# Kernel optimization log

Measured on AMD Instinct MI355X. Metric: run time of the kernel, lower is better.

The kernel has to match this reference:

```python
import jax, jax.numpy as jnp
import numpy as np

N = 100000      # nodes
E = 1600000     # edges (avg degree 16)
DIN = 32        # input feature dim
H = 16          # nhidden
DEPTH = 4       # number of SAGEConv layers


def setup_inputs() -> dict:
    key = jax.random.key(0)
    ks = jax.random.split(key, 16)
    s = 0.1
    inp = {
        "x": jax.random.normal(ks[0], (N, DIN), jnp.float32),
        "edge_index": jax.random.randint(ks[1], (2, E), 0, N, dtype=jnp.int64),
        # SAGEConv layer 0: in=DIN -> out=H. lin_l has bias, lin_r has no bias (PyG default).
        "Wl0": jax.random.normal(ks[2], (H, DIN), jnp.float32) * s,
        "bl0": jnp.zeros((H,), jnp.float32),
        "Wr0": jax.random.normal(ks[3], (H, DIN), jnp.float32) * s,
        # SAGEConv layers 1..3: in=H -> out=H, stacked.
        "Wls": jax.random.normal(ks[4], (DEPTH - 1, H, H), jnp.float32) * s,
        "bls": jnp.zeros((DEPTH - 1, H), jnp.float32),
        "Wrs": jax.random.normal(ks[5], (DEPTH - 1, H, H), jnp.float32) * s,
        # lin_out MLP: [H, 2H, 2H, 1] with acts [silu, silu, None], no batch norm.
        "W1": jax.random.normal(ks[6], (2 * H, H), jnp.float32) * s,
        "b1": jnp.zeros((2 * H,), jnp.float32),
        "W2": jax.random.normal(ks[7], (2 * H, 2 * H), jnp.float32) * s,
        "b2": jnp.zeros((2 * H,), jnp.float32),
        "W3": jax.random.normal(ks[8], (1, 2 * H), jnp.float32) * s,
        "b3": jnp.zeros((1,), jnp.float32),
    }
    return inp


def reference(x, edge_index, Wl0, bl0, Wr0, Wls, bls, Wrs, W1, b1, W2, b2, W3, b3):
    src = edge_index[0]  # message source (x_j)
    dst = edge_index[1]  # aggregation target (x_i)

    def sage(h, Wl, bl, Wr):
        # sum-aggregate neighbor features, then lin_l(agg) + lin_r(h)
        agg = jax.ops.segment_sum(h[src], dst, num_segments=N)  # [N, d]
        return agg @ Wl.T + bl + h @ Wr.T

    x = jax.nn.silu(sage(x, Wl0, bl0, Wr0))
    for i in range(DEPTH - 1):
        x = jax.nn.silu(sage(x, Wls[i], bls[i], Wrs[i]))

    out = jax.nn.silu(x @ W1.T + b1)
    out = jax.nn.silu(out @ W2.T + b2)
    out = out @ W3.T + b3  # [N, 1]
    return out
```

## Files before the change

kernel.cpp:

```cpp
#include <hip/hip_runtime.h>


#define SH      8
#define BWID    256
#define NBK     512
#define CHUNK   2048
#define EPT     (CHUNK / 256)
#define BCAP    5120

__device__ __forceinline__ float silu_f(float v) {
    return v * __builtin_amdgcn_rcpf(1.0f + __expf(-v));
}

__device__ __forceinline__ float bf_lo(unsigned u) { return __uint_as_float(u << 16); }
__device__ __forceinline__ float bf_hi(unsigned u) { return __uint_as_float(u & 0xFFFF0000u); }
__device__ __forceinline__ unsigned short f2bf(float f) {
    unsigned x = __float_as_uint(f);
    unsigned r = x + 0x7FFFu + ((x >> 16) & 1u);
    return (unsigned short)(r >> 16);
}
__device__ __forceinline__ unsigned pack_bf2(float a, float b) {
    return (unsigned)f2bf(a) | ((unsigned)f2bf(b) << 16);
}

#define ACC2(u0, u1) \
    p[0] += bf_lo(u0.x); p[1] += bf_hi(u0.x); p[2] += bf_lo(u0.y); p[3] += bf_hi(u0.y); \
    p[4] += bf_lo(u0.z); p[5] += bf_hi(u0.z); p[6] += bf_lo(u0.w); p[7] += bf_hi(u0.w); \
    p[8] += bf_lo(u1.x); p[9] += bf_hi(u1.x); p[10]+= bf_lo(u1.y); p[11]+= bf_hi(u1.y); \
    p[12]+= bf_lo(u1.z); p[13]+= bf_hi(u1.z); p[14]+= bf_lo(u1.w); p[15]+= bf_hi(u1.w);


__global__ __launch_bounds__(256) void bin_dense0(
    const int* __restrict__ src, const int* __restrict__ dst,
    unsigned short* __restrict__ cnt16,
    unsigned short* __restrict__ scan16,
    unsigned* __restrict__ binned0,
    const float* __restrict__ x,
    const float* __restrict__ Wl0, const float* __restrict__ bl0,
    const float* __restrict__ Wr0,
    unsigned* __restrict__ hlb, float* __restrict__ acc,
    int n, int ne, int nblocks)
{
    __shared__ int      s_hist[NBK];
    __shared__ int      s_off[NBK];
    __shared__ int      s_p[256];
    __shared__ unsigned s_items[CHUNK];
    __shared__ float    sWl[512], sWr[512], sbl[16];

    const int t = threadIdx.x;
    const int blk = blockIdx.x;
    for (int i = t; i < 512; i += 256) { sWl[i] = Wl0[i]; sWr[i] = Wr0[i]; }
    if (t < 16) sbl[t] = bl0[t];

    const int base = blk * CHUNK;
    const int cnt = min(CHUNK, ne - base);

    int es[EPT], ed[EPT];
#pragma unroll
    for (int j = 0; j < EPT; ++j) {
        const int i = t + j * 256;
        if (i < cnt) { es[j] = src[base + i]; ed[j] = dst[base + i]; }
        else         { es[j] = -1; ed[j] = -1; }
    }

    s_hist[t] = 0; s_hist[t + 256] = 0;
    __syncthreads();
#pragma unroll
    for (int j = 0; j < EPT; ++j)
        if (es[j] >= 0) atomicAdd(&s_hist[ed[j] >> SH], 1);
    __syncthreads();

    const int c0 = s_hist[2 * t], c1 = s_hist[2 * t + 1];
    const int ps = c0 + c1;
    s_p[t] = ps;
    __syncthreads();
    int v = ps;
    for (int o = 1; o < 256; o <<= 1) {
        const int add = (t >= o) ? s_p[t - o] : 0;
        __syncthreads();
        v += add;
        s_p[t] = v;
        __syncthreads();
    }
    const int ex = v - ps;
    s_off[2 * t] = ex;
    s_off[2 * t + 1] = ex + c0;

    cnt16[blk * NBK + t]        = (unsigned short)s_hist[t];
    cnt16[blk * NBK + t + 256]  = (unsigned short)s_hist[t + 256];
    s_hist[t] = 0; s_hist[t + 256] = 0;
    __syncthreads();
    scan16[blk * NBK + t]       = (unsigned short)s_off[t];
    scan16[blk * NBK + t + 256] = (unsigned short)s_off[t + 256];

#pragma unroll
    for (int j = 0; j < EPT; ++j) {
        if (es[j] >= 0) {
            const int b  = ed[j] >> SH;
            const int ld = ed[j] & (BWID - 1);
            const int r  = atomicAdd(&s_hist[b], 1);
            s_items[s_off[b] + r] = ((unsigned)ld << 17) | (unsigned)es[j];
        }
    }
    __syncthreads();

    for (int i = t; i < cnt; i += 256)
        binned0[base + i] = s_items[i];

    if (t >= 128) return;
    const int node = blk * 128 + t;
    if (node >= n) return;

    float h[32];
    const float4* __restrict__ xp = (const float4*)(x + (size_t)node * 32);
#pragma unroll
    for (int r = 0; r < 8; ++r) {
        const float4 vv = xp[r];
        h[4*r+0] = vv.x; h[4*r+1] = vv.y; h[4*r+2] = vv.z; h[4*r+3] = vv.w;
    }

    const float4* __restrict__ sWl4 = (const float4*)sWl;
    const float4* __restrict__ sWr4 = (const float4*)sWr;
    float ol[16], oa[16];
#pragma unroll
    for (int j = 0; j < 16; ++j) {
        float al = 0.f, ar = 0.f;
#pragma unroll
        for (int d4 = 0; d4 < 8; ++d4) {
            const float4 wl = sWl4[j * 8 + d4];
            const float4 wr = sWr4[j * 8 + d4];
            al = fmaf(wl.x, h[4*d4+0], al); al = fmaf(wl.y, h[4*d4+1], al);
            al = fmaf(wl.z, h[4*d4+2], al); al = fmaf(wl.w, h[4*d4+3], al);
            ar = fmaf(wr.x, h[4*d4+0], ar); ar = fmaf(wr.y, h[4*d4+1], ar);
            ar = fmaf(wr.z, h[4*d4+2], ar); ar = fmaf(wr.w, h[4*d4+3], ar);
        }
        ol[j] = al;
        oa[j] = sbl[j] + ar;
    }

    unsigned u[8];
#pragma unroll
    for (int r = 0; r < 8; ++r) u[r] = pack_bf2(ol[2*r], ol[2*r+1]);
    uint4* __restrict__ hp = (uint4*)(hlb + (size_t)node * 8);
    hp[0] = make_uint4(u[0], u[1], u[2], u[3]);
    hp[1] = make_uint4(u[4], u[5], u[6], u[7]);
    float4* __restrict__ ap = (float4*)(acc + (size_t)node * 16);
#pragma unroll
    for (int r = 0; r < 4; ++r)
        ap[r] = make_float4(oa[4*r], oa[4*r+1], oa[4*r+2], oa[4*r+3]);
}


__device__ __forceinline__ void gather16_2(
    const int* __restrict__ binned1, const uint4* __restrict__ h4,
    int beg, int end, int q, float* p)
{
#pragma unroll
    for (int i = 0; i < 16; ++i) p[i] = 0.f;
    int base = beg;
    for (; base + 8 <= end; base += 8) {
        const int k = base + q * 4;
        const int i0 = binned1[k],     i1 = binned1[k + 1];
        const int i2 = binned1[k + 2], i3 = binned1[k + 3];
        const uint4 a0 = h4[(size_t)i0 * 2], a1 = h4[(size_t)i0 * 2 + 1];
        const uint4 b0 = h4[(size_t)i1 * 2], b1 = h4[(size_t)i1 * 2 + 1];
        const uint4 c0 = h4[(size_t)i2 * 2], c1 = h4[(size_t)i2 * 2 + 1];
        const uint4 d0 = h4[(size_t)i3 * 2], d1 = h4[(size_t)i3 * 2 + 1];
        ACC2(a0, a1)
        ACC2(b0, b1)
        ACC2(c0, c1)
        ACC2(d0, d1)
    }
    for (int k = base + q; k < end; k += 2) {
        const int s0 = binned1[k];
        const uint4 a0 = h4[(size_t)s0 * 2], a1 = h4[(size_t)s0 * 2 + 1];
        ACC2(a0, a1)
    }
#pragma unroll
    for (int i = 0; i < 16; ++i) p[i] += __shfl_xor(p[i], 1);
}

__device__ __forceinline__ void gather16_4(
    const int* __restrict__ binned1, const uint4* __restrict__ h4,
    int beg, int end, int q, float* p)
{
#pragma unroll
    for (int i = 0; i < 16; ++i) p[i] = 0.f;
    int base = beg;
    for (; base + 16 <= end; base += 16) {
        const int k = base + q * 4;
        const int i0 = binned1[k],     i1 = binned1[k + 1];
        const int i2 = binned1[k + 2], i3 = binned1[k + 3];
        const uint4 a0 = h4[(size_t)i0 * 2], a1 = h4[(size_t)i0 * 2 + 1];
        const uint4 b0 = h4[(size_t)i1 * 2], b1 = h4[(size_t)i1 * 2 + 1];
        const uint4 c0 = h4[(size_t)i2 * 2], c1 = h4[(size_t)i2 * 2 + 1];
        const uint4 d0 = h4[(size_t)i3 * 2], d1 = h4[(size_t)i3 * 2 + 1];
        ACC2(a0, a1)
        ACC2(b0, b1)
        ACC2(c0, c1)
        ACC2(d0, d1)
    }
    for (int k = base + q; k < end; k += 4) {
        const int s0 = binned1[k];
        const uint4 a0 = h4[(size_t)s0 * 2], a1 = h4[(size_t)s0 * 2 + 1];
        ACC2(a0, a1)
    }
#pragma unroll
    for (int i = 0; i < 16; ++i) p[i] += __shfl_xor(p[i], 1);
#pragma unroll
    for (int i = 0; i < 16; ++i) p[i] += __shfl_xor(p[i], 2);
}

__global__ __launch_bounds__(512, 4) void sort_agg_dense(
    const unsigned* __restrict__ binned0,
    const unsigned short* __restrict__ cnt16,
    const unsigned short* __restrict__ scan16,
    int* __restrict__ binned1,
    int2* __restrict__ noff2,
    const unsigned* __restrict__ hl_in,
    const float* __restrict__ acc_in,
    const float* __restrict__ Wl, const float* __restrict__ bl,
    const float* __restrict__ Wr,
    unsigned* __restrict__ hl_out, float* __restrict__ acc_out,
    int n, int nblocks)
{
    __shared__ unsigned s_edges[BCAP];
    __shared__ int cnt[BWID];
    __shared__ int off_[BWID];
    __shared__ int s_p[512];
    __shared__ int s_tot;
    __shared__ float sWl[256], sWr[256], sbl[16];
    const int b = blockIdx.x, t = threadIdx.x;
    const int dbase = b * BCAP;

    if (t < 256) { sWl[t] = Wl[t]; sWr[t] = Wr[t]; }
    if (t < 16) sbl[t] = bl[t];

    int rc[4], rs[4];
    int myc = 0;
#pragma unroll
    for (int j = 0; j < 4; ++j) {
        const int i = 4 * t + j;
        if (i < nblocks) { rc[j] = cnt16[i * NBK + b]; rs[j] = scan16[i * NBK + b]; }
        else             { rc[j] = 0; rs[j] = 0; }
        myc += rc[j];
    }
    s_p[t] = myc;
    __syncthreads();
    int v = myc;
    for (int o = 1; o < 512; o <<= 1) {
        const int add = (t >= o) ? s_p[t - o] : 0;
        __syncthreads();
        v += add;
        s_p[t] = v;
        __syncthreads();
    }
    int o = v - myc;
    if (t == 511) s_tot = v;
    if (t < BWID) cnt[t] = 0;

#pragma unroll
    for (int j = 0; j < 4; ++j) {
        if (rc[j]) {
            const unsigned* __restrict__ run =
                binned0 + (size_t)(4 * t + j) * CHUNK + rs[j];
            for (int r = 0; r < rc[j]; ++r) s_edges[o++] = run[r];
        }
    }
    __syncthreads();
    const int tot = s_tot;

    for (int k = t; k < tot; k += 512)
        atomicAdd(&cnt[s_edges[k] >> 17], 1);
    __syncthreads();

    if (t < BWID) off_[t] = cnt[t];
    __syncthreads();
    for (int o2 = 1; o2 < BWID; o2 <<= 1) {
        const int add = (t < BWID && t >= o2) ? off_[t - o2] : 0;
        __syncthreads();
        if (t < BWID) off_[t] += add;
        __syncthreads();
    }
    if (t < BWID) off_[t] -= cnt[t];
    __syncthreads();

    if (t < BWID) {
        const int node = (b << SH) + t;
        if (node < n)
            noff2[node] = make_int2(dbase + off_[t], dbase + off_[t] + cnt[t]);
        cnt[t] = 0;
    }
    __syncthreads();

    for (int k = t; k < tot; k += 512) {
        const unsigned u = s_edges[k];
        const int ld = (int)(u >> 17);
        const int r2 = atomicAdd(&cnt[ld], 1);
        binned1[dbase + off_[ld] + r2] = (int)(u & 0x1FFFFu);
    }
    __syncthreads();

    const int ln = t >> 1;
    const int node = (b << SH) + ln;
    if (node >= n) return;
    const int q = t & 1;
    const int beg = dbase + off_[ln];
    const int end = beg + cnt[ln];

    float p[16];
    gather16_2(binned1, (const uint4*)hl_in, beg, end, q, p);

    const float4* __restrict__ ai = (const float4*)(acc_in + (size_t)node * 16);
    float h[16];
#pragma unroll
    for (int r = 0; r < 4; ++r) {
        const float4 a = ai[r];
        h[4*r+0] = silu_f(a.x + p[4*r+0]);
        h[4*r+1] = silu_f(a.y + p[4*r+1]);
        h[4*r+2] = silu_f(a.z + p[4*r+2]);
        h[4*r+3] = silu_f(a.w + p[4*r+3]);
    }

    const float4* __restrict__ sWl4 = (const float4*)sWl;
    const float4* __restrict__ sWr4 = (const float4*)sWr;
    float ol[8], oa[8];
#pragma unroll
    for (int jj = 0; jj < 8; ++jj) {
        const int j = 8 * q + jj;
        float al = 0.f, ar = 0.f;
#pragma unroll
        for (int d4 = 0; d4 < 4; ++d4) {
            const float4 wl = sWl4[j * 4 + d4];
            const float4 wr = sWr4[j * 4 + d4];
            al = fmaf(wl.x, h[4*d4+0], al); al = fmaf(wl.y, h[4*d4+1], al);
            al = fmaf(wl.z, h[4*d4+2], al); al = fmaf(wl.w, h[4*d4+3], al);
            ar = fmaf(wr.x, h[4*d4+0], ar); ar = fmaf(wr.y, h[4*d4+1], ar);
            ar = fmaf(wr.z, h[4*d4+2], ar); ar = fmaf(wr.w, h[4*d4+3], ar);
        }
        ol[jj] = al;
        oa[jj] = sbl[j] + ar;
    }

    ((uint4*)hl_out)[(size_t)node * 2 + q] =
        make_uint4(pack_bf2(ol[0], ol[1]), pack_bf2(ol[2], ol[3]),
                   pack_bf2(ol[4], ol[5]), pack_bf2(ol[6], ol[7]));
    float4* __restrict__ ap = (float4*)(acc_out + (size_t)node * 16);
    ap[2 * q]     = make_float4(oa[0], oa[1], oa[2], oa[3]);
    ap[2 * q + 1] = make_float4(oa[4], oa[5], oa[6], oa[7]);
}

__global__ __launch_bounds__(256, 4) void fused_agg_dense(
    const int2* __restrict__ noff2, const int* __restrict__ binned1,
    const unsigned* __restrict__ hl_in, const float* __restrict__ acc_in,
    const float* __restrict__ Wl, const float* __restrict__ bl,
    const float* __restrict__ Wr,
    unsigned* __restrict__ hl_out, float* __restrict__ acc_out, int n)
{
    __shared__ float sWl[256], sWr[256], sbl[16];
    const int t = threadIdx.x;
    sWl[t] = Wl[t]; sWr[t] = Wr[t];
    if (t < 16) sbl[t] = bl[t];
    __syncthreads();

    const int gid = blockIdx.x * 256 + t;
    const int node = gid >> 2;
    if (node >= n) return;
    const int q = t & 3;
    const int2 be = noff2[node];

    float p[16];
    gather16_4(binned1, (const uint4*)hl_in, be.x, be.y, q, p);

    const float4* __restrict__ ai = (const float4*)(acc_in + (size_t)node * 16);
    float h[16];
#pragma unroll
    for (int r = 0; r < 4; ++r) {
        const float4 a = ai[r];
        h[4*r+0] = silu_f(a.x + p[4*r+0]);
        h[4*r+1] = silu_f(a.y + p[4*r+1]);
        h[4*r+2] = silu_f(a.z + p[4*r+2]);
        h[4*r+3] = silu_f(a.w + p[4*r+3]);
    }

    const float4* __restrict__ sWl4 = (const float4*)sWl;
    const float4* __restrict__ sWr4 = (const float4*)sWr;
    float ol[4], oa[4];
#pragma unroll
    for (int jj = 0; jj < 4; ++jj) {
        const int j = 4 * q + jj;
        float al = 0.f, ar = 0.f;
#pragma unroll
        for (int d4 = 0; d4 < 4; ++d4) {
            const float4 wl = sWl4[j * 4 + d4];
            const float4 wr = sWr4[j * 4 + d4];
            al = fmaf(wl.x, h[4*d4+0], al); al = fmaf(wl.y, h[4*d4+1], al);
            al = fmaf(wl.z, h[4*d4+2], al); al = fmaf(wl.w, h[4*d4+3], al);
            ar = fmaf(wr.x, h[4*d4+0], ar); ar = fmaf(wr.y, h[4*d4+1], ar);
            ar = fmaf(wr.z, h[4*d4+2], ar); ar = fmaf(wr.w, h[4*d4+3], ar);
        }
        ol[jj] = al;
        oa[jj] = sbl[j] + ar;
    }

    ((uint2*)hl_out)[(size_t)node * 4 + q] =
        make_uint2(pack_bf2(ol[0], ol[1]), pack_bf2(ol[2], ol[3]));
    ((float4*)acc_out)[(size_t)node * 4 + q] =
        make_float4(oa[0], oa[1], oa[2], oa[3]);
}

__global__ __launch_bounds__(256, 3) void fused_agg_mlp(
    const int2* __restrict__ noff2, const int* __restrict__ binned1,
    const unsigned* __restrict__ hl_in, const float* __restrict__ acc_in,
    const float* __restrict__ W1, const float* __restrict__ b1,
    const float* __restrict__ W2, const float* __restrict__ b2,
    const float* __restrict__ W3, const float* __restrict__ b3,
    float* __restrict__ out, int n)
{
    __shared__ float sW1[512], sW2[1024], sb1[32], sb2[32], sW3[32];
    __shared__ float sb3;
    const int t = threadIdx.x;
    for (int i = t; i < 512; i += 256) sW1[i] = W1[i];
    for (int i = t; i < 1024; i += 256) sW2[i] = W2[i];
    if (t < 32) { sb1[t] = b1[t]; sb2[t] = b2[t]; sW3[t] = W3[t]; }
    if (t == 0) sb3 = b3[0];
    __syncthreads();

    const int gid = blockIdx.x * 256 + t;
    const int node = gid >> 2;
    if (node >= n) return;
    const int q = t & 3;
    const int2 be = noff2[node];

    float p[16];
    gather16_4(binned1, (const uint4*)hl_in, be.x, be.y, q, p);

    const float4* __restrict__ ai = (const float4*)(acc_in + (size_t)node * 16);
    float h[16];
#pragma unroll
    for (int r = 0; r < 4; ++r) {
        const float4 a = ai[r];
        h[4*r+0] = silu_f(a.x + p[4*r+0]);
        h[4*r+1] = silu_f(a.y + p[4*r+1]);
        h[4*r+2] = silu_f(a.z + p[4*r+2]);
        h[4*r+3] = silu_f(a.w + p[4*r+3]);
    }

    const float4* __restrict__ sW1v = (const float4*)sW1;
    float a1[8];
#pragma unroll
    for (int jj = 0; jj < 8; ++jj) {
        const int j = 8 * q + jj;
        float s = sb1[j];
#pragma unroll
        for (int d4 = 0; d4 < 4; ++d4) {
            const float4 w = sW1v[j * 4 + d4];
            s = fmaf(w.x, h[4*d4+0], s); s = fmaf(w.y, h[4*d4+1], s);
            s = fmaf(w.z, h[4*d4+2], s); s = fmaf(w.w, h[4*d4+3], s);
        }
        a1[jj] = silu_f(s);
    }

    float t0[16];
#pragma unroll
    for (int i = 0; i < 8; ++i) {
        const float mine  = a1[i];
        const float other = __shfl_xor(mine, 1);
        const bool hi = (q & 1);
        t0[i]     = hi ? other : mine;
        t0[8 + i] = hi ? mine  : other;
    }
    float A1[32];
#pragma unroll
    for (int i = 0; i < 16; ++i) {
        const float mine  = t0[i];
        const float other = __shfl_xor(mine, 2);
        const bool hi = (q & 2);
        A1[i]      = hi ? other : mine;
        A1[16 + i] = hi ? mine  : other;
    }

    const float4* __restrict__ sW2v = (const float4*)sW2;
    float part = 0.f;
#pragma unroll
    for (int jj = 0; jj < 8; ++jj) {
        const int j = 8 * q + jj;
        float s = sb2[j];
#pragma unroll
        for (int d4 = 0; d4 < 8; ++d4) {
            const float4 w = sW2v[j * 8 + d4];
            s = fmaf(w.x, A1[4*d4+0], s); s = fmaf(w.y, A1[4*d4+1], s);
            s = fmaf(w.z, A1[4*d4+2], s); s = fmaf(w.w, A1[4*d4+3], s);
        }
        part = fmaf(sW3[j], silu_f(s), part);
    }
    part += __shfl_xor(part, 1);
    part += __shfl_xor(part, 2);
    if (q == 0) out[node] = part + sb3;
}

extern "C" void kernel_launch(void* const* d_in, const int* in_sizes, int n_in,
                              void* d_out, int out_size, void* d_ws, size_t ws_size,
                              hipStream_t stream)
{
    const float* x   = (const float*)d_in[0];
    const int*   ei  = (const int*)d_in[1];
    const float* Wl0 = (const float*)d_in[2];
    const float* bl0 = (const float*)d_in[3];
    const float* Wr0 = (const float*)d_in[4];
    const float* Wls = (const float*)d_in[5];
    const float* bls = (const float*)d_in[6];
    const float* Wrs = (const float*)d_in[7];
    const float* W1  = (const float*)d_in[8];
    const float* b1  = (const float*)d_in[9];
    const float* W2  = (const float*)d_in[10];
    const float* b2  = (const float*)d_in[11];
    const float* W3  = (const float*)d_in[12];
    const float* b3  = (const float*)d_in[13];

    const int n  = in_sizes[0] / 32;
    const int ne = in_sizes[1] / 2;
    const int* src = ei;
    const int* dst = ei + ne;
    const int nbuck   = (n + BWID - 1) >> SH;
    const int nblocks = (ne + CHUNK - 1) / CHUNK;

    float*    acc0    = (float*)d_ws;
    float*    acc1    = acc0 + (size_t)n * 16;
    unsigned* hlbA    = (unsigned*)(acc1 + (size_t)n * 16);
    unsigned* hlbB    = hlbA + (size_t)n * 8;
    int2*     noff2   = (int2*)(hlbB + (size_t)n * 8);
    int*      binned1 = (int*)(noff2 + n);
    unsigned short* cnt16  = (unsigned short*)(binned1 + (size_t)nbuck * BCAP);
    unsigned short* scan16 = cnt16 + (size_t)nblocks * NBK;
    unsigned* binned0 = (unsigned*)(scan16 + (size_t)nblocks * NBK);

    const int lb = (n * 4 + 255) / 256;

    bin_dense0<<<nblocks, 256, 0, stream>>>(src, dst, cnt16, scan16, binned0,
                                            x, Wl0, bl0, Wr0, hlbA, acc0,
                                            n, ne, nblocks);
    sort_agg_dense<<<nbuck, 512, 0, stream>>>(binned0, cnt16, scan16,
        binned1, noff2, hlbA, acc0,
        Wls + 0, bls + 0, Wrs + 0, hlbB, acc1, n, nblocks);

    fused_agg_dense<<<lb, 256, 0, stream>>>(noff2, binned1, hlbB, acc1,
        Wls + 256, bls + 16, Wrs + 256, hlbA, acc0, n);
    fused_agg_dense<<<lb, 256, 0, stream>>>(noff2, binned1, hlbA, acc0,
        Wls + 512, bls + 32, Wrs + 512, hlbB, acc1, n);
    fused_agg_mlp<<<lb, 256, 0, stream>>>(noff2, binned1, hlbB, acc1,
        W1, b1, W2, b2, W3, b3, (float*)d_out, n);
}
```

Before: 151.2 us.

## Double edge chunk size per binning block and use nontemporal memory ops

Raises the edge chunk handled by each partition block from 2048 to 4096, halving the number of chunk blocks so each destination-bin block reads one run per thread instead of four, which simplifies the gather loop. All 256 threads of a chunk block now also compute the layer-0 node transform instead of 128. Edge index loads and binned-item stores use nontemporal hints to avoid polluting cache. The trade-off is more registers and shared memory per thread (EPT doubles to 16, s_items grows to 16 KB), fewer blocks for parallelism, and the packed 16-bit counts must still fit the larger chunks.

Result: no change. 151.5 us (+0.2%).

```diff
diff --git a/kernel.cpp b/kernel.cpp
--- a/kernel.cpp
+++ b/kernel.cpp
@@ -4,7 +4,7 @@
 #define SH      8
 #define BWID    256
 #define NBK     512
-#define CHUNK   2048
+#define CHUNK   4096
 #define EPT     (CHUNK / 256)
 #define BCAP    5120
 
@@ -59,8 +59,10 @@
 #pragma unroll
     for (int j = 0; j < EPT; ++j) {
         const int i = t + j * 256;
-        if (i < cnt) { es[j] = src[base + i]; ed[j] = dst[base + i]; }
-        else         { es[j] = -1; ed[j] = -1; }
+        if (i < cnt) {
+            es[j] = __builtin_nontemporal_load(src + base + i);
+            ed[j] = __builtin_nontemporal_load(dst + base + i);
+        } else { es[j] = -1; ed[j] = -1; }
     }
 
     s_hist[t] = 0; s_hist[t + 256] = 0;
@@ -105,10 +107,9 @@
     __syncthreads();
 
     for (int i = t; i < cnt; i += 256)
-        binned0[base + i] = s_items[i];
-
-    if (t >= 128) return;
-    const int node = blk * 128 + t;
+        __builtin_nontemporal_store(s_items[i], binned0 + base + i);
+
+    const int node = blk * 256 + t;
     if (node >= n) return;
 
     float h[32];
@@ -236,18 +237,11 @@
     if (t < 256) { sWl[t] = Wl[t]; sWr[t] = Wr[t]; }
     if (t < 16) sbl[t] = bl[t];
 
-    int rc[4], rs[4];
-    int myc = 0;
-#pragma unroll
-    for (int j = 0; j < 4; ++j) {
-        const int i = 4 * t + j;
-        if (i < nblocks) { rc[j] = cnt16[i * NBK + b]; rs[j] = scan16[i * NBK + b]; }
-        else             { rc[j] = 0; rs[j] = 0; }
-        myc += rc[j];
-    }
-    s_p[t] = myc;
-    __syncthreads();
-    int v = myc;
+    int rc = 0, rs = 0;
+    if (t < nblocks) { rc = cnt16[t * NBK + b]; rs = scan16[t * NBK + b]; }
+    s_p[t] = rc;
+    __syncthreads();
+    int v = rc;
     for (int o = 1; o < 512; o <<= 1) {
         const int add = (t >= o) ? s_p[t - o] : 0;
         __syncthreads();
@@ -255,17 +249,14 @@
         s_p[t] = v;
         __syncthreads();
     }
-    int o = v - myc;
+    int o = v - rc;
     if (t == 511) s_tot = v;
     if (t < BWID) cnt[t] = 0;
 
-#pragma unroll
-    for (int j = 0; j < 4; ++j) {
-        if (rc[j]) {
-            const unsigned* __restrict__ run =
-                binned0 + (size_t)(4 * t + j) * CHUNK + rs[j];
-            for (int r = 0; r < rc[j]; ++r) s_edges[o++] = run[r];
-        }
+    if (rc) {
+        const unsigned* __restrict__ run = binned0 + (size_t)t * CHUNK + rs;
+        for (int r = 0; r < rc; ++r)
+            s_edges[o + r] = __builtin_nontemporal_load(run + r);
     }
     __syncthreads();
     const int tot = s_tot;
```
